# Kernel optimization log

Measured on AMD Instinct MI355X. Metric: run time of the kernel, lower is better.

## Reference

```python
import jax, jax.numpy as jnp
import numpy as np

B, N, INDIM = 512, 200, 200
D1, D2, D3 = 32, 32, 8
RATIO = 0.5
K1 = int(np.ceil(RATIO * N))    # 100 nodes kept after pool1
K2 = int(np.ceil(RATIO * K1))   # 50 nodes kept after pool2
BN_EPS = 1e-5
NEG = -1e9


def setup_inputs() -> dict:
    key = jax.random.key(0)
    ks = jax.random.split(key, 16)
    x = jax.random.normal(ks[0], (B, N, INDIM), jnp.float32)
    u = jax.random.uniform(ks[1], (B, N, N), jnp.float32)
    ut = jnp.triu(jnp.where(u > 0.9, u, 0.0), 1)
    adj = ut + jnp.swapaxes(ut, 1, 2)
    g = lambda i, shape: jax.random.normal(ks[i], shape, jnp.float32) * 0.1
    return dict(
        x=x, adj=adj,
        W1=g(2, (INDIM, D1)), a1s=g(3, (D1,)), a1d=g(4, (D1,)), b1=jnp.zeros((D1,), jnp.float32),
        W2=g(5, (D1, D2)), a2s=g(6, (D2,)), a2d=g(7, (D2,)), b2=jnp.zeros((D2,), jnp.float32),
        pw1=g(8, (D1,)), pw2=g(9, (D2,)),
        fc1_w=g(10, ((D1 + D2) * 2, D2)), fc1_b=jnp.zeros((D2,), jnp.float32),
        fc2_w=g(11, (D2, D3)), fc2_b=jnp.zeros((D3,), jnp.float32),
        fc3_w=g(12, (D3, 2)), fc3_b=jnp.zeros((2,), jnp.float32),
        bn4_g=jnp.ones((D2,), jnp.float32), bn4_b=jnp.zeros((D2,), jnp.float32),
        bn5_g=jnp.ones((D3,), jnp.float32), bn5_b=jnp.zeros((D3,), jnp.float32))


def _gat(x, mask, W, a_s, a_d, b):
    # PyG GATConv (heads=1): alpha_ij = softmax_j LeakyReLU(a_d.h_i + a_s.h_j) over in-neighbors j (self-loops added)
    h = jnp.einsum('bnf,fd->bnd', x, W)
    es = h @ a_s                    # [B,n] source term
    ed = h @ a_d                    # [B,n] dest term
    m = mask | jnp.eye(mask.shape[1], dtype=bool)
    logits = jax.nn.leaky_relu(ed[:, :, None] + es[:, None, :], 0.2)
    alpha = jax.nn.softmax(jnp.where(m, logits, NEG), axis=-1)   # [B,n,n]
    return jnp.einsum('bij,bjd->bid', alpha, h) + b


def _topk(x, adj_w, w, k):
    # TopKPooling(multiplier=1, nonlinearity=sigmoid): score = sigmoid(x.w/||w||)
    score = jax.nn.sigmoid((x @ w) / (jnp.linalg.norm(w) + 1e-16))   # [B,n]
    vals, idx = jax.lax.top_k(score, k)                              # perm sorted desc, as PyG
    xk = jnp.take_along_axis(x, idx[:, :, None], axis=1) * vals[:, :, None]
    ak = jnp.take_along_axis(jnp.take_along_axis(adj_w, idx[:, :, None], axis=1), idx[:, None, :], axis=2)
    return xk, ak, vals


def _bn(z, g, b):
    # eval-mode BatchNorm1d: running_mean=0, running_var=1
    return g * z / jnp.sqrt(1.0 + BN_EPS) + b


def reference(x, adj, W1, a1s, a1d, b1, W2, a2s, a2d, b2, pw1, pw2,
              fc1_w, fc1_b, fc2_w, fc2_b, fc3_w, fc3_b, bn4_g, bn4_b, bn5_g, bn5_b):
    h = _gat(x, adj > 0, W1, a1s, a1d, b1)
    h, aw, s1 = _topk(h, adj, pw1, K1)
    x1 = jnp.concatenate([h.max(axis=1), h.mean(axis=1)], axis=1)    # [B, 64]
    # augment_adj: add self-loops, spspmm (A+I)@(A+I), remove self-loops
    eye = jnp.eye(K1, dtype=aw.dtype)
    a2 = jnp.einsum('bij,bjk->bik', aw + eye, aw + eye) * (1.0 - eye)
    h = _gat(h, a2 != 0, W2, a2s, a2d, b2)
    h, _, s2 = _topk(h, a2, pw2, K2)
    x2 = jnp.concatenate([h.max(axis=1), h.mean(axis=1)], axis=1)    # [B, 64]
    z = jnp.concatenate([x1, x2], axis=1)                            # [B, 128]
    z = _bn(jax.nn.relu(z @ fc1_w + fc1_b), bn4_g, bn4_b)            # dropout: eval -> identity
    z = _bn(jax.nn.relu(z @ fc2_w + fc2_b), bn5_g, bn5_b)
    logp = jax.nn.log_softmax(z @ fc3_w + fc3_b, axis=-1)            # [B, 2]
    return logp, s1, s2
```

## Files before the change

### kernel.cpp

```cpp
#include <hip/hip_runtime.h>
#include <math.h>

#define N_    200
#define B_    512
#define K1_   100
#define K2_   50
#define ST    36
#define NBCAP 128

#define S1_OFF 1024
#define S2_OFF 52224

__device__ __forceinline__ float lrelu(float v) { return v > 0.f ? v : 0.2f * v; }
__device__ __forceinline__ float sigm(float v)  { return 1.f / (1.f + __expf(-v)); }


__global__ __launch_bounds__(256) void gnn_fused(
    const float* __restrict__ x, const float* __restrict__ adj,
    const float* __restrict__ W1, const float* __restrict__ a1s,
    const float* __restrict__ a1d, const float* __restrict__ b1,
    const float* __restrict__ W2g, const float* __restrict__ a2s,
    const float* __restrict__ a2d, const float* __restrict__ b2,
    const float* __restrict__ pw1, const float* __restrict__ pw2,
    const float* __restrict__ fc1w, const float* __restrict__ fc1b,
    const float* __restrict__ fc2w, const float* __restrict__ fc2b,
    const float* __restrict__ fc3w, const float* __restrict__ fc3b,
    const float* __restrict__ bn4g, const float* __restrict__ bn4b,
    const float* __restrict__ bn5g, const float* __restrict__ bn5b,
    float* __restrict__ out)
{
  __shared__ __align__(16) char smem[65968];
  float*         sH    = (float*)smem;
  float*         sXK   = sH + 100 * ST;
  unsigned*      sBITS = (unsigned*)(smem + 28800);
  float*         sW2   = (float*)(smem + 28800);
  unsigned char* sNbr  = (unsigned char*)(smem + 34400);
  float*         sES   = (float*)(smem + 60000);
  float*         sED   = (float*)(smem + 60800);
  float*         sKey  = (float*)(smem + 61600);
  int*           sSel  = (int*)(smem + 62624);
  float*         sVal  = (float*)(smem + 63024);
  float*         sXV   = (float*)(smem + 63424);
  float*         sRed  = (float*)(smem + 63936);
  unsigned*      sMask2= (unsigned*)(smem + 63968);

  const int t = threadIdx.x;
  const int b = blockIdx.x;
  const float* xb = x   + (size_t)b * N_ * N_;
  const float* ab = adj + (size_t)b * N_ * N_;

  if (t < N_) {
    float acc[32];
    #pragma unroll
    for (int d = 0; d < 32; ++d) acc[d] = 0.f;
    const float* xr = xb + t * N_;
    for (int k = 0; k < N_; k += 4) {
      float4 xv = *(const float4*)(xr + k);
      #pragma unroll
      for (int kk = 0; kk < 4; ++kk) {
        float xs = (&xv.x)[kk];
        const float* wr = W1 + (k + kk) * 32;
        #pragma unroll
        for (int d = 0; d < 32; ++d) acc[d] += xs * wr[d];
      }
    }
    float es = 0.f, ed = 0.f;
    #pragma unroll
    for (int d = 0; d < 32; ++d) { es += acc[d] * a1s[d]; ed += acc[d] * a1d[d]; }
    sES[t] = es; sED[t] = ed;
    #pragma unroll
    for (int d = 0; d < 32; ++d) sH[t * ST + d] = acc[d];
  }
  __syncthreads();

  {
    float v = (t < N_) ? sES[t] : -3.0e38f;
    #pragma unroll
    for (int off = 1; off < 64; off <<= 1) v = fmaxf(v, __shfl_xor(v, off, 64));
    if ((t & 63) == 0) sRed[t >> 6] = v;
  }
  __syncthreads();
  {
    float esmax = fmaxf(fmaxf(sRed[0], sRed[1]), fmaxf(sRed[2], sRed[3]));

    float acc[32];
    if (t < N_) {
      const float* arow = ab + (size_t)t * N_;
      unsigned char* nl = sNbr + t * NBCAP;
      int cnt = 0;
      for (int jw = 0; jw < 7; ++jw) {
        int jbase = jw * 32;
        int lim = (jw < 6) ? 32 : 8;
        unsigned mb = 0u;
        for (int j4 = 0; j4 < lim; j4 += 4) {
          float4 av = *(const float4*)(arow + jbase + j4);
          #pragma unroll
          for (int jj = 0; jj < 4; ++jj) {
            int j = jbase + j4 + jj;
            bool conn = (&av.x)[jj] > 0.f;
            if (conn) mb |= 1u << (j4 + jj);
            if (conn || j == t) nl[cnt++] = (unsigned char)j;
          }
        }
        sBITS[t * 7 + jw] = mb;
      }
      float ed_i = sED[t];
      float L = lrelu(ed_i + esmax);
      float ssum = 0.f;
      #pragma unroll
      for (int d = 0; d < 32; ++d) acc[d] = 0.f;
      for (int i = 0; i < cnt; ++i) {
        int j = nl[i];
        float w = __expf(lrelu(ed_i + sES[j]) - L);
        ssum += w;
        const float* hr = &sH[j * ST];
        #pragma unroll
        for (int c = 0; c < 8; ++c) {
          float4 hv = *(const float4*)(hr + c * 4);
          acc[c * 4 + 0] += w * hv.x;
          acc[c * 4 + 1] += w * hv.y;
          acc[c * 4 + 2] += w * hv.z;
          acc[c * 4 + 3] += w * hv.w;
        }
      }
      float inv = 1.f / ssum;
      #pragma unroll
      for (int d = 0; d < 32; ++d) acc[d] = acc[d] * inv + b1[d];
    }
    __syncthreads();
    if (t < N_) {
      #pragma unroll
      for (int d = 0; d < 32; ++d) sH[t * ST + d] = acc[d];
    }
  }
  __syncthreads();

  {
    float npw = 0.f;
    #pragma unroll
    for (int d = 0; d < 32; ++d) npw += pw1[d] * pw1[d];
    npw = sqrtf(npw) + 1e-16f;
    float sc = -1.f;
    if (t < N_) {
      float dp = 0.f;
      #pragma unroll
      for (int d = 0; d < 32; ++d) dp += sH[t * ST + d] * pw1[d];
      sc = sigm(dp / npw);
    }
    sKey[t] = sc;
  }
  __syncthreads();
  if (t < N_) {
    float sc = sKey[t];
    int rank = 0;
    for (int j = 0; j < N_; j += 4) {
      #pragma unroll
      for (int jj = 0; jj < 4; ++jj) {
        float o = sKey[j + jj];
        rank += (o > sc || (o == sc && (j + jj) < t)) ? 1 : 0;
      }
    }
    if (rank < K1_) {
      sSel[rank] = t; sVal[rank] = sc;
      out[S1_OFF + b * K1_ + rank] = sc;
    }
  }
  __syncthreads();
  {
    float tmp[13];
    #pragma unroll
    for (int it = 0; it < 13; ++it) {
      int i = t + it * 256;
      if (i < K1_ * 32) tmp[it] = sH[sSel[i >> 5] * ST + (i & 31)] * sVal[i >> 5];
    }
    __syncthreads();
    #pragma unroll
    for (int it = 0; it < 13; ++it) {
      int i = t + it * 256;
      if (i < K1_ * 32) sXK[(i >> 5) * ST + (i & 31)] = tmp[it];
    }
  }
  __syncthreads();
  if (t < 32) {
    float m = -3.0e38f, s = 0.f;
    for (int r = 0; r < K1_; ++r) { float v = sXK[r * ST + t]; m = fmaxf(m, v); s += v; }
    sXV[t] = m; sXV[32 + t] = s / 100.f;
  }

  if (t < K1_) {
    int gi = sSel[t];
    #pragma unroll
    for (int w = 0; w < 4; ++w) {
      unsigned m = 0;
      const int lim = (w < 3) ? 32 : 4;
      for (int jj = 0; jj < lim; ++jj) {
        int j = w * 32 + jj;
        int gj = sSel[j];
        unsigned bit = (sBITS[gi * 7 + (gj >> 5)] >> (gj & 31)) & 1u;
        if (j == t) bit = 1u;
        m |= bit << jj;
      }
      sMask2[t * 5 + w] = m;
    }
  }
  __syncthreads();
  for (int i = t; i < 1024; i += 256) sW2[i] = W2g[i];
  {
    unsigned pr0 = 0, pr1 = 0, pr2 = 0, pr3 = 0;
    if (t < K1_) {
      #pragma unroll
      for (int kw = 0; kw < 4; ++kw) {
        unsigned mk = sMask2[t * 5 + kw];
        const int lim = (kw < 3) ? 32 : 4;
        for (int kk = 0; kk < lim; ++kk) {
          if ((mk >> kk) & 1u) {
            int k = kw * 32 + kk;
            pr0 |= sMask2[k * 5 + 0]; pr1 |= sMask2[k * 5 + 1];
            pr2 |= sMask2[k * 5 + 2]; pr3 |= sMask2[k * 5 + 3];
          }
        }
      }
    }
    __syncthreads();
    if (t < K1_) {
      sMask2[t * 5 + 0] = pr0; sMask2[t * 5 + 1] = pr1;
      sMask2[t * 5 + 2] = pr2; sMask2[t * 5 + 3] = pr3;
    }
  }
  __syncthreads();

  if (t < K1_) {
    float xk[32];
    #pragma unroll
    for (int c = 0; c < 8; ++c) *(float4*)&xk[c * 4] = *(const float4*)&sXK[t * ST + c * 4];
    float acc[32];
    #pragma unroll
    for (int d = 0; d < 32; ++d) acc[d] = 0.f;
    #pragma unroll
    for (int k = 0; k < 32; ++k) {
      float xv = xk[k];
      const float* wr = &sW2[k * 32];
      #pragma unroll
      for (int d = 0; d < 32; ++d) acc[d] += xv * wr[d];
    }
    float es = 0.f, ed = 0.f;
    #pragma unroll
    for (int d = 0; d < 32; ++d) { es += acc[d] * a2s[d]; ed += acc[d] * a2d[d]; }
    sES[t] = es; sED[t] = ed;
    #pragma unroll
    for (int d = 0; d < 32; ++d) sH[t * ST + d] = acc[d];
  }
  __syncthreads();
  {
    float v = (t < K1_) ? sES[t] : -3.0e38f;
    #pragma unroll
    for (int off = 1; off < 64; off <<= 1) v = fmaxf(v, __shfl_xor(v, off, 64));
    if ((t & 63) == 0) sRed[t >> 6] = v;
  }
  __syncthreads();
  {
    float esm2 = fmaxf(fmaxf(sRed[0], sRed[1]), fmaxf(sRed[2], sRed[3]));
    float acc[32];
    if (t < K1_) {
      float ed_i = sED[t];
      float L = lrelu(ed_i + esm2);
      float ssum = 0.f;
      #pragma unroll
      for (int d = 0; d < 32; ++d) acc[d] = 0.f;
      #pragma unroll
      for (int jw = 0; jw < 4; ++jw) {
        unsigned mw = sMask2[t * 5 + jw];
        const int lim = (jw < 3) ? 32 : 4;
        for (int jj = 0; jj < lim; ++jj) {
          int j = jw * 32 + jj;
          float w = 0.f;
          if ((mw >> jj) & 1u) w = __expf(lrelu(ed_i + sES[j]) - L);
          ssum += w;
          const float* hr = &sH[j * ST];
          #pragma unroll
          for (int d = 0; d < 32; ++d) acc[d] += w * hr[d];
        }
      }
      float inv = 1.f / ssum;
      #pragma unroll
      for (int d = 0; d < 32; ++d) acc[d] = acc[d] * inv + b2[d];
    }
    __syncthreads();
    if (t < K1_) {
      #pragma unroll
      for (int d = 0; d < 32; ++d) sH[t * ST + d] = acc[d];
    }
  }
  __syncthreads();

  {
    float npw = 0.f;
    #pragma unroll
    for (int d = 0; d < 32; ++d) npw += pw2[d] * pw2[d];
    npw = sqrtf(npw) + 1e-16f;
    if (t < K1_) {
      float dp = 0.f;
      #pragma unroll
      for (int d = 0; d < 32; ++d) dp += sH[t * ST + d] * pw2[d];
      sKey[t] = sigm(dp / npw);
    }
  }
  __syncthreads();
  if (t < K1_) {
    float sc = sKey[t];
    int rank = 0;
    for (int j = 0; j < K1_; j += 4) {
      #pragma unroll
      for (int jj = 0; jj < 4; ++jj) {
        float o = sKey[j + jj];
        rank += (o > sc || (o == sc && (j + jj) < t)) ? 1 : 0;
      }
    }
    if (rank < K2_) {
      sSel[rank] = t; sVal[rank] = sc;
      out[S2_OFF + b * K2_ + rank] = sc;
    }
  }
  __syncthreads();
  {
    int d = t & 31, r0 = t >> 5;
    for (int r = r0; r < K2_; r += 8) sXK[r * ST + d] = sH[sSel[r] * ST + d] * sVal[r];
  }
  __syncthreads();
  if (t < 32) {
    float m = -3.0e38f, s = 0.f;
    for (int r = 0; r < K2_; ++r) { float v = sXK[r * ST + t]; m = fmaxf(m, v); s += v; }
    sXV[64 + t] = m; sXV[96 + t] = s / 50.f;
  }
  __syncthreads();

  const float RS = 0.99999500003749969f;
  if (t < 32) {
    float z = fc1b[t];
    for (int k = 0; k < 128; ++k) z += sXV[k] * fc1w[k * 32 + t];
    z = fmaxf(z, 0.f);
    z = bn4g[t] * z * RS + bn4b[t];
    sKey[t] = z;
  }
  __syncthreads();
  if (t < 8) {
    float z = fc2b[t];
    for (int k = 0; k < 32; ++k) z += sKey[k] * fc2w[k * 8 + t];
    z = fmaxf(z, 0.f);
    z = bn5g[t] * z * RS + bn5b[t];
    sKey[32 + t] = z;
  }
  __syncthreads();
  if (t < 2) {
    float z = fc3b[t];
    for (int k = 0; k < 8; ++k) z += sKey[32 + k] * fc3w[k * 2 + t];
    sKey[40 + t] = z;
  }
  __syncthreads();
  if (t < 2) {
    float z0 = sKey[40], z1 = sKey[41];
    float m = fmaxf(z0, z1);
    float lse = m + logf(__expf(z0 - m) + __expf(z1 - m));
    out[b * 2 + t] = sKey[40 + t] - lse;
  }
}

extern "C" void kernel_launch(void* const* d_in, const int* in_sizes, int n_in,
                              void* d_out, int out_size, void* d_ws, size_t ws_size,
                              hipStream_t stream) {
  (void)in_sizes; (void)n_in; (void)d_ws; (void)ws_size; (void)out_size;
  const float* x    = (const float*)d_in[0];
  const float* adj  = (const float*)d_in[1];
  const float* W1   = (const float*)d_in[2];
  const float* a1s  = (const float*)d_in[3];
  const float* a1d  = (const float*)d_in[4];
  const float* b1   = (const float*)d_in[5];
  const float* W2   = (const float*)d_in[6];
  const float* a2s  = (const float*)d_in[7];
  const float* a2d  = (const float*)d_in[8];
  const float* b2   = (const float*)d_in[9];
  const float* pw1  = (const float*)d_in[10];
  const float* pw2  = (const float*)d_in[11];
  const float* fc1w = (const float*)d_in[12];
  const float* fc1b = (const float*)d_in[13];
  const float* fc2w = (const float*)d_in[14];
  const float* fc2b = (const float*)d_in[15];
  const float* fc3w = (const float*)d_in[16];
  const float* fc3b = (const float*)d_in[17];
  const float* bn4g = (const float*)d_in[18];
  const float* bn4b = (const float*)d_in[19];
  const float* bn5g = (const float*)d_in[20];
  const float* bn5b = (const float*)d_in[21];

  gnn_fused<<<B_, 256, 0, stream>>>(x, adj, W1, a1s, a1d, b1, W2, a2s, a2d, b2,
                                    pw1, pw2, fc1w, fc1b, fc2w, fc2b, fc3w, fc3b,
                                    bn4g, bn4b, bn5g, bn5b, (float*)d_out);
}
```

Before: 339.9 us.

## Stage x tiles through double-buffered LDS and build adjacency bitmasks with wave ballots

The first GAT projection now streams x in 20-column K-tiles through a double-buffered LDS region using coalesced float4 loads prefetched into registers, replacing per-thread strided row reads. While the tiles are in flight, each wave reads adjacency rows coalesced and builds neighbor bitmasks with __ballot, and the per-thread neighbor byte list is removed. Aggregation now walks those bitmasks with ctz, and the W2 load is moved earlier. In exchange, the kernel uses more LDS, adds barriers per tile, and the bitmask stride changes from 7 to 8 words.

```diff
diff --git a/kernel.cpp b/kernel.cpp
--- a/kernel.cpp
+++ b/kernel.cpp
@@ -6,7 +6,9 @@
 #define K1_   100
 #define K2_   50
 #define ST    36
-#define NBCAP 128
+#define XS    21
+#define KT    20
+#define NT    10
 
 #define S1_OFF 1024
 #define S2_OFF 52224
@@ -29,41 +31,119 @@
     const float* __restrict__ bn5g, const float* __restrict__ bn5b,
     float* __restrict__ out)
 {
-  __shared__ __align__(16) char smem[65968];
-  float*         sH    = (float*)smem;
-  float*         sXK   = sH + 100 * ST;
-  unsigned*      sBITS = (unsigned*)(smem + 28800);
-  float*         sW2   = (float*)(smem + 28800);
-  unsigned char* sNbr  = (unsigned char*)(smem + 34400);
-  float*         sES   = (float*)(smem + 60000);
-  float*         sED   = (float*)(smem + 60800);
-  float*         sKey  = (float*)(smem + 61600);
-  int*           sSel  = (int*)(smem + 62624);
-  float*         sVal  = (float*)(smem + 63024);
-  float*         sXV   = (float*)(smem + 63424);
-  float*         sRed  = (float*)(smem + 63936);
-  unsigned*      sMask2= (unsigned*)(smem + 63968);
-
-  const int t = threadIdx.x;
-  const int b = blockIdx.x;
+  __shared__ __align__(16) char smem[72768];
+  float*    sXs   = (float*)smem;
+  float*    sW2   = (float*)smem;
+  unsigned* sMask2= (unsigned*)(smem + 4096);
+  float*    sH    = (float*)(smem + 33600);
+  float*    sXK   = sH + 100 * ST;
+  unsigned* sBITS = (unsigned*)(smem + 62400);
+  float*    sES   = (float*)(smem + 68800);
+  float*    sED   = (float*)(smem + 69600);
+  float*    sKey  = (float*)(smem + 70400);
+  int*      sSel  = (int*)(smem + 71424);
+  float*    sVal  = (float*)(smem + 71824);
+  float*    sXV   = (float*)(smem + 72224);
+  float*    sRed  = (float*)(smem + 72736);
+
+  const int t  = threadIdx.x;
+  const int b  = blockIdx.x;
+  const int wv = t >> 6, ln = t & 63;
   const float* xb = x   + (size_t)b * N_ * N_;
   const float* ab = adj + (size_t)b * N_ * N_;
+  const float4* xb4 = (const float4*)xb;
+
+  float acc[32];
+  #pragma unroll
+  for (int d = 0; d < 32; ++d) acc[d] = 0.f;
+
+  float4 q0, q1, q2, q3;
+  {
+    int f0 = t,        r0 = f0 / 5, c0 = f0 % 5;
+    int f1 = t + 256,  r1 = f1 / 5, c1 = f1 % 5;
+    int f2 = t + 512,  r2 = f2 / 5, c2 = f2 % 5;
+    int f3 = t + 768,  r3 = f3 / 5, c3 = f3 % 5;
+    q0 = xb4[r0 * 50 + c0];
+    q1 = xb4[r1 * 50 + c1];
+    q2 = xb4[r2 * 50 + c2];
+    if (f3 < 1000) q3 = xb4[r3 * 50 + c3];
+    float* d0 = sXs + r0 * XS + c0 * 4; d0[0]=q0.x; d0[1]=q0.y; d0[2]=q0.z; d0[3]=q0.w;
+    float* d1 = sXs + r1 * XS + c1 * 4; d1[0]=q1.x; d1[1]=q1.y; d1[2]=q1.z; d1[3]=q1.w;
+    float* d2 = sXs + r2 * XS + c2 * 4; d2[0]=q2.x; d2[1]=q2.y; d2[2]=q2.z; d2[3]=q2.w;
+    if (f3 < 1000) { float* d3 = sXs + r3 * XS + c3 * 4; d3[0]=q3.x; d3[1]=q3.y; d3[2]=q3.z; d3[3]=q3.w; }
+  }
+  __syncthreads();
+
+  int cur = 0;
+  for (int it = 0; it < NT; ++it) {
+    if (it + 1 < NT) {
+      int kb4 = (it + 1) * (KT / 4);
+      int f0 = t,       r0 = f0 / 5, c0 = f0 % 5;
+      int f1 = t + 256, r1 = f1 / 5, c1 = f1 % 5;
+      int f2 = t + 512, r2 = f2 / 5, c2 = f2 % 5;
+      int f3 = t + 768, r3 = f3 / 5, c3 = f3 % 5;
+      q0 = xb4[r0 * 50 + kb4 + c0];
+      q1 = xb4[r1 * 50 + kb4 + c1];
+      q2 = xb4[r2 * 50 + kb4 + c2];
+      if (f3 < 1000) q3 = xb4[r3 * 50 + kb4 + c3];
+    }
+    {
+      int rbase = wv * 50 + it * 5;
+      for (int rr = 0; rr < 5; ++rr) {
+        int row = rbase + rr;
+        const float* arow = ab + row * N_;
+        float a0 = arow[ln];
+        float a1 = arow[64 + ln];
+        float a2 = arow[128 + ln];
+        float a3 = (ln < 8) ? arow[192 + ln] : -1.f;
+        unsigned long long b0 = __ballot(a0 > 0.f);
+        unsigned long long b1 = __ballot(a1 > 0.f);
+        unsigned long long b2 = __ballot(a2 > 0.f);
+        unsigned long long b3 = __ballot(a3 > 0.f);
+        if (ln == 0) {
+          sBITS[row * 8 + 0] = (unsigned)b0; sBITS[row * 8 + 1] = (unsigned)(b0 >> 32);
+          sBITS[row * 8 + 2] = (unsigned)b1; sBITS[row * 8 + 3] = (unsigned)(b1 >> 32);
+          sBITS[row * 8 + 4] = (unsigned)b2; sBITS[row * 8 + 5] = (unsigned)(b2 >> 32);
+          sBITS[row * 8 + 6] = (unsigned)b3;
+        }
+      }
+    }
+    if (t < N_) {
+      const float* xr = sXs + cur * 4200 + t * XS;
+      const int k0 = it * KT;
+      for (int k = 0; k < KT; k += 4) {
+        float x0 = xr[k], x1 = xr[k + 1], x2 = xr[k + 2], x3 = xr[k + 3];
+        const float* w0 = W1 + (k0 + k) * 32;
+        const float* w1 = w0 + 32;
+        const float* w2 = w0 + 64;
+        const float* w3 = w0 + 96;
+        #pragma unroll
+        for (int d = 0; d < 32; ++d) acc[d] += x0 * w0[d];
+        #pragma unroll
+        for (int d = 0; d < 32; ++d) acc[d] += x1 * w1[d];
+        #pragma unroll
+        for (int d = 0; d < 32; ++d) acc[d] += x2 * w2[d];
+        #pragma unroll
+        for (int d = 0; d < 32; ++d) acc[d] += x3 * w3[d];
+      }
+    }
+    __syncthreads();
+    if (it + 1 < NT) {
+      float* B = sXs + (cur ^ 1) * 4200;
+      int f0 = t,       r0 = f0 / 5, c0 = f0 % 5;
+      int f1 = t + 256, r1 = f1 / 5, c1 = f1 % 5;
+      int f2 = t + 512, r2 = f2 / 5, c2 = f2 % 5;
+      int f3 = t + 768, r3 = f3 / 5, c3 = f3 % 5;
+      float* d0 = B + r0 * XS + c0 * 4; d0[0]=q0.x; d0[1]=q0.y; d0[2]=q0.z; d0[3]=q0.w;
+      float* d1 = B + r1 * XS + c1 * 4; d1[0]=q1.x; d1[1]=q1.y; d1[2]=q1.z; d1[3]=q1.w;
+      float* d2 = B + r2 * XS + c2 * 4; d2[0]=q2.x; d2[1]=q2.y; d2[2]=q2.z; d2[3]=q2.w;
+      if (f3 < 1000) { float* d3 = B + r3 * XS + c3 * 4; d3[0]=q3.x; d3[1]=q3.y; d3[2]=q3.z; d3[3]=q3.w; }
+      __syncthreads();
+    }
+    cur ^= 1;
+  }
 
   if (t < N_) {
-    float acc[32];
-    #pragma unroll
-    for (int d = 0; d < 32; ++d) acc[d] = 0.f;
-    const float* xr = xb + t * N_;
-    for (int k = 0; k < N_; k += 4) {
-      float4 xv = *(const float4*)(xr + k);
-      #pragma unroll
-      for (int kk = 0; kk < 4; ++kk) {
-        float xs = (&xv.x)[kk];
-        const float* wr = W1 + (k + kk) * 32;
-        #pragma unroll
-        for (int d = 0; d < 32; ++d) acc[d] += xs * wr[d];
-      }
-    }
     float es = 0.f, ed = 0.f;
     #pragma unroll
     for (int d = 0; d < 32; ++d) { es += acc[d] * a1s[d]; ed += acc[d] * a1d[d]; }
@@ -73,6 +153,7 @@
   }
   __syncthreads();
 
+  for (int i = t; i < 1024; i += 256) sW2[i] = W2g[i];
   {
     float v = (t < N_) ? sES[t] : -3.0e38f;
     #pragma unroll
@@ -83,46 +164,34 @@
   {
     float esmax = fmaxf(fmaxf(sRed[0], sRed[1]), fmaxf(sRed[2], sRed[3]));
 
-    float acc[32];
     if (t < N_) {
-      const float* arow = ab + (size_t)t * N_;
-      unsigned char* nl = sNbr + t * NBCAP;
-      int cnt = 0;
-      for (int jw = 0; jw < 7; ++jw) {
-        int jbase = jw * 32;
-        int lim = (jw < 6) ? 32 : 8;
-        unsigned mb = 0u;
-        for (int j4 = 0; j4 < lim; j4 += 4) {
-          float4 av = *(const float4*)(arow + jbase + j4);
-          #pragma unroll
-          for (int jj = 0; jj < 4; ++jj) {
-            int j = jbase + j4 + jj;
-            bool conn = (&av.x)[jj] > 0.f;
-            if (conn) mb |= 1u << (j4 + jj);
-            if (conn || j == t) nl[cnt++] = (unsigned char)j;
-          }
-        }
-        sBITS[t * 7 + jw] = mb;
-      }
+      unsigned long long m0 = (unsigned long long)sBITS[t * 8 + 0] | ((unsigned long long)sBITS[t * 8 + 1] << 32);
+      unsigned long long m1 = (unsigned long long)sBITS[t * 8 + 2] | ((unsigned long long)sBITS[t * 8 + 3] << 32);
+      unsigned long long m2 = (unsigned long long)sBITS[t * 8 + 4] | ((unsigned long long)sBITS[t * 8 + 5] << 32);
+      unsigned long long m3 = (unsigned long long)sBITS[t * 8 + 6];
+      if (t < 64)       m0 |= 1ull << t;
+      else if (t < 128) m1 |= 1ull << (t - 64);
+      else if (t < 192) m2 |= 1ull << (t - 128);
+      else              m3 |= 1ull << (t - 192);
       float ed_i = sED[t];
       float L = lrelu(ed_i + esmax);
       float ssum = 0.f;
       #pragma unroll
       for (int d = 0; d < 32; ++d) acc[d] = 0.f;
-      for (int i = 0; i < cnt; ++i) {
-        int j = nl[i];
-        float w = __expf(lrelu(ed_i + sES[j]) - L);
-        ssum += w;
-        const float* hr = &sH[j * ST];
-        #pragma unroll
-        for (int c = 0; c < 8; ++c) {
-          float4 hv = *(const float4*)(hr + c * 4);
-          acc[c * 4 + 0] += w * hv.x;
-          acc[c * 4 + 1] += w * hv.y;
-          acc[c * 4 + 2] += w * hv.z;
-          acc[c * 4 + 3] += w * hv.w;
+      #define AGG(mm, base)                                                        \
+        while (mm) {                                                               \
+          int j = (base) + (int)__builtin_ctzll(mm); mm &= (mm - 1);               \
+          float w = __expf(lrelu(ed_i + sES[j]) - L); ssum += w;                   \
+          const float* hr = &sH[j * ST];                                           \
+          _Pragma("unroll")                                                        \
+          for (int c = 0; c < 8; ++c) {                                            \
+            float4 hv = *(const float4*)(hr + c * 4);                              \
+            acc[c*4+0] += w * hv.x; acc[c*4+1] += w * hv.y;                        \
+            acc[c*4+2] += w * hv.z; acc[c*4+3] += w * hv.w;                        \
+          }                                                                        \
         }
-      }
+      AGG(m0, 0) AGG(m1, 64) AGG(m2, 128) AGG(m3, 192)
+      #undef AGG
       float inv = 1.f / ssum;
       #pragma unroll
       for (int d = 0; d < 32; ++d) acc[d] = acc[d] * inv + b1[d];
@@ -196,7 +265,7 @@
       for (int jj = 0; jj < lim; ++jj) {
         int j = w * 32 + jj;
         int gj = sSel[j];
-        unsigned bit = (sBITS[gi * 7 + (gj >> 5)] >> (gj & 31)) & 1u;
+        unsigned bit = (sBITS[gi * 8 + (gj >> 5)] >> (gj & 31)) & 1u;
         if (j == t) bit = 1u;
         m |= bit << jj;
       }
@@ -204,7 +273,6 @@
     }
   }
   __syncthreads();
-  for (int i = t; i < 1024; i += 256) sW2[i] = W2g[i];
   {
     unsigned pr0 = 0, pr1 = 0, pr2 = 0, pr3 = 0;
     if (t < K1_) {
@@ -233,22 +301,22 @@
     float xk[32];
     #pragma unroll
     for (int c = 0; c < 8; ++c) *(float4*)&xk[c * 4] = *(const float4*)&sXK[t * ST + c * 4];
-    float acc[32];
-    #pragma unroll
-    for (int d = 0; d < 32; ++d) acc[d] = 0.f;
+    float acc2[32];
+    #pragma unroll
+    for (int d = 0; d < 32; ++d) acc2[d] = 0.f;
     #pragma unroll
     for (int k = 0; k < 32; ++k) {
       float xv = xk[k];
       const float* wr = &sW2[k * 32];
       #pragma unroll
-      for (int d = 0; d < 32; ++d) acc[d] += xv * wr[d];
+      for (int d = 0; d < 32; ++d) acc2[d] += xv * wr[d];
     }
     float es = 0.f, ed = 0.f;
     #pragma unroll
-    for (int d = 0; d < 32; ++d) { es += acc[d] * a2s[d]; ed += acc[d] * a2d[d]; }
+    for (int d = 0; d < 32; ++d) { es += acc2[d] * a2s[d]; ed += acc2[d] * a2d[d]; }
     sES[t] = es; sED[t] = ed;
     #pragma unroll
-    for (int d = 0; d < 32; ++d) sH[t * ST + d] = acc[d];
+    for (int d = 0; d < 32; ++d) sH[t * ST + d] = acc2[d];
   }
   __syncthreads();
   {
@@ -260,13 +328,13 @@
   __syncthreads();
   {
     float esm2 = fmaxf(fmaxf(sRed[0], sRed[1]), fmaxf(sRed[2], sRed[3]));
-    float acc[32];
+    float acc2[32];
     if (t < K1_) {
       float ed_i = sED[t];
       float L = lrelu(ed_i + esm2);
       float ssum = 0.f;
       #pragma unroll
-      for (int d = 0; d < 32; ++d) acc[d] = 0.f;
+      for (int d = 0; d < 32; ++d) acc2[d] = 0.f;
       #pragma unroll
       for (int jw = 0; jw < 4; ++jw) {
         unsigned mw = sMask2[t * 5 + jw];
@@ -278,17 +346,17 @@
           ssum += w;
           const float* hr = &sH[j * ST];
           #pragma unroll
-          for (int d = 0; d < 32; ++d) acc[d] += w * hr[d];
+          for (int d = 0; d < 32; ++d) acc2[d] += w * hr[d];
         }
       }
       float inv = 1.f / ssum;
       #pragma unroll
-      for (int d = 0; d < 32; ++d) acc[d] = acc[d] * inv + b2[d];
+      for (int d = 0; d < 32; ++d) acc2[d] = acc2[d] * inv + b2[d];
     }
     __syncthreads();
     if (t < K1_) {
       #pragma unroll
-      for (int d = 0; d < 32; ++d) sH[t * ST + d] = acc[d];
+      for (int d = 0; d < 32; ++d) sH[t * ST + d] = acc2[d];
     }
   }
   __syncthreads();
```

Result: no change. 343.7 us (+1.1%).
